# Performance work log

Measured on AMD Instinct MI355X. Metric: run time of the kernel, lower is better.

The kernel has to match this reference:

```python
import jax, jax.numpy as jnp
import numpy as np

N_NODES = 100000
IN_FEAT = 256
OUT_FEAT = 128
N_EDGES = 3200000


def setup_inputs() -> dict:
    key = jax.random.key(0)
    k1, k2, k3, k4, k5 = jax.random.split(key, 5)
    inputs = jax.random.normal(k1, (N_NODES, IN_FEAT), dtype=jnp.float32)
    # xavier-uniform-like init for weight
    limit = float(np.sqrt(6.0 / (IN_FEAT + OUT_FEAT)))
    weight = jax.random.uniform(k2, (IN_FEAT, OUT_FEAT), dtype=jnp.float32, minval=-limit, maxval=limit)
    adj_rows = jnp.sort(jax.random.randint(k3, (N_EDGES,), 0, N_NODES, dtype=jnp.int64))
    adj_cols = jax.random.randint(k4, (N_EDGES,), 0, N_NODES, dtype=jnp.int64)
    adj_vals = jax.random.uniform(k5, (N_EDGES,), dtype=jnp.float32)
    return {"inputs": inputs, "weight": weight, "adj_rows": adj_rows,
            "adj_cols": adj_cols, "adj_vals": adj_vals}


def reference(inputs, weight, adj_rows, adj_cols, adj_vals):
    # support = X @ W  -> [N, out_features]
    support = jnp.matmul(inputs, weight)
    # output = spmm(A, support): out[r] += vals[e] * support[cols[e]] for row r = rows[e]
    gathered = adj_vals[:, None] * support[adj_cols]  # [E, out_features]
    output = jax.ops.segment_sum(gathered, adj_rows, num_segments=N_NODES)
    return output
```

## Files before the change

kernel.cpp:

```cpp
#include <hip/hip_runtime.h>

#define IN_FEAT 256
#define OUT_FEAT 128

typedef __attribute__((ext_vector_type(8))) short bf16x8;
typedef __attribute__((ext_vector_type(4))) float f32x4;

static __device__ __forceinline__ unsigned short f2bf(float f) {
    union { float f; unsigned u; } v; v.f = f;
    unsigned u = v.u;
    return (unsigned short)((u + 0x7FFFu + ((u >> 16) & 1u)) >> 16);
}
static __device__ __forceinline__ float bfl(unsigned u) {
    union { unsigned u; float f; } x; x.u = u << 16; return x.f;
}
static __device__ __forceinline__ float bfh(unsigned u) {
    union { unsigned u; float f; } x; x.u = u & 0xFFFF0000u; return x.f;
}

__global__ __launch_bounds__(256) void prep_wt(const float* __restrict__ W,
                                               unsigned short* __restrict__ Wt) {
    int idx = blockIdx.x * 256 + threadIdx.x;
    int n = idx >> 8, k = idx & 255;
    Wt[idx] = f2bf(W[(size_t)k * OUT_FEAT + n]);
}

__global__ __launch_bounds__(256) void rowptr_kernel(const int* __restrict__ rows,
                                                     int* __restrict__ row_ptr,
                                                     int E, int N) {
    int i = blockIdx.x * 256 + threadIdx.x;
    if (i > N) return;
    int lo = 0, hi = E;
    while (lo < hi) {
        int mid = (lo + hi) >> 1;
        if (rows[mid] < i) lo = mid + 1; else hi = mid;
    }
    row_ptr[i] = lo;
}

__global__ __launch_bounds__(256) void gemm_bf16(const float* __restrict__ X,
                                                 const unsigned short* __restrict__ Wt,
                                                 unsigned short* __restrict__ S, int M) {
    __shared__ unsigned short As[128 * 64];
    __shared__ unsigned short Bs[128 * 64];

    const int t = threadIdx.x;
    const int m0 = blockIdx.x * 128;
    const int lane = t & 63;
    const int w = t >> 6;
    const int wm = w >> 1, wn = w & 1;
    const int lr = lane & 15, lg = lane >> 4;

    f32x4 acc[4][4];
#pragma unroll
    for (int mi = 0; mi < 4; ++mi)
#pragma unroll
        for (int ni = 0; ni < 4; ++ni)
            acc[mi][ni] = (f32x4){0.f, 0.f, 0.f, 0.f};

    const int r_st = t >> 1;
    const int h_st = t & 1;

    for (int k0 = 0; k0 < IN_FEAT; k0 += 64) {
        int gr = m0 + r_st; if (gr >= M) gr = M - 1;
        const float4* xp = (const float4*)(X + (size_t)gr * IN_FEAT + k0 + h_st * 32);
#pragma unroll
        for (int j = 0; j < 4; ++j) {
            float4 f0 = xp[2 * j], f1 = xp[2 * j + 1];
            uint4 pk;
            pk.x = (unsigned)f2bf(f0.x) | ((unsigned)f2bf(f0.y) << 16);
            pk.y = (unsigned)f2bf(f0.z) | ((unsigned)f2bf(f0.w) << 16);
            pk.z = (unsigned)f2bf(f1.x) | ((unsigned)f2bf(f1.y) << 16);
            pk.w = (unsigned)f2bf(f1.z) | ((unsigned)f2bf(f1.w) << 16);
            int s = h_st * 4 + j;
            *(uint4*)((char*)As + r_st * 128 + ((s ^ (r_st & 7)) << 4)) = pk;
        }
        const uint4* wp = (const uint4*)(Wt + (size_t)r_st * 256 + k0 + h_st * 32);
#pragma unroll
        for (int j = 0; j < 4; ++j) {
            uint4 pk = wp[j];
            int s = h_st * 4 + j;
            *(uint4*)((char*)Bs + r_st * 128 + ((s ^ (r_st & 7)) << 4)) = pk;
        }
        __syncthreads();

#pragma unroll
        for (int kb = 0; kb < 2; ++kb) {
            const int sb = kb * 4 + lg;
            bf16x8 a[4], b[4];
#pragma unroll
            for (int mi = 0; mi < 4; ++mi) {
                int r = wm * 64 + mi * 16 + lr;
                a[mi] = *(const bf16x8*)((const char*)As + r * 128 + ((sb ^ (r & 7)) << 4));
            }
#pragma unroll
            for (int ni = 0; ni < 4; ++ni) {
                int r = wn * 64 + ni * 16 + lr;
                b[ni] = *(const bf16x8*)((const char*)Bs + r * 128 + ((sb ^ (r & 7)) << 4));
            }
#pragma unroll
            for (int mi = 0; mi < 4; ++mi)
#pragma unroll
                for (int ni = 0; ni < 4; ++ni)
                    acc[mi][ni] = __builtin_amdgcn_mfma_f32_16x16x32_bf16(a[mi], b[ni], acc[mi][ni], 0, 0, 0);
        }
        __syncthreads();
    }

#pragma unroll
    for (int mi = 0; mi < 4; ++mi) {
#pragma unroll
        for (int j = 0; j < 4; ++j) {
            int row = m0 + wm * 64 + mi * 16 + lg * 4 + j;
            if (row < M) {
#pragma unroll
                for (int ni = 0; ni < 4; ++ni) {
                    int col = wn * 64 + ni * 16 + lr;
                    S[(size_t)row * OUT_FEAT + col] = f2bf(acc[mi][ni][j]);
                }
            }
        }
    }
}

__global__ __launch_bounds__(256) void spmm_bf16(const int* __restrict__ cols,
                                                 const float* __restrict__ vals,
                                                 const unsigned short* __restrict__ S,
                                                 const int* __restrict__ row_ptr,
                                                 float* __restrict__ out, int N) {
    const int w = threadIdx.x >> 6;
    const int lane = threadIdx.x & 63;
    const int r = blockIdx.x * 4 + w;
    if (r >= N) return;
    const int g = lane >> 4;
    const int fb = lane & 15;
    const int start = row_ptr[r], end = row_ptr[r + 1];

    float acc[8] = {0.f, 0.f, 0.f, 0.f, 0.f, 0.f, 0.f, 0.f};
    const unsigned short* Sb = S + fb * 8;

    for (int base = start; base < end; base += 8) {
        int e0 = base + g;
        int e1 = base + 4 + g;
        if (e0 < end) {
            int c = cols[e0]; float v = vals[e0];
            uint4 p = *(const uint4*)(Sb + (size_t)c * OUT_FEAT);
            acc[0] += v * bfl(p.x); acc[1] += v * bfh(p.x);
            acc[2] += v * bfl(p.y); acc[3] += v * bfh(p.y);
            acc[4] += v * bfl(p.z); acc[5] += v * bfh(p.z);
            acc[6] += v * bfl(p.w); acc[7] += v * bfh(p.w);
        }
        if (e1 < end) {
            int c = cols[e1]; float v = vals[e1];
            uint4 p = *(const uint4*)(Sb + (size_t)c * OUT_FEAT);
            acc[0] += v * bfl(p.x); acc[1] += v * bfh(p.x);
            acc[2] += v * bfl(p.y); acc[3] += v * bfh(p.y);
            acc[4] += v * bfl(p.z); acc[5] += v * bfh(p.z);
            acc[6] += v * bfl(p.w); acc[7] += v * bfh(p.w);
        }
    }

#pragma unroll
    for (int j = 0; j < 8; ++j) {
        acc[j] += __shfl_xor(acc[j], 16);
        acc[j] += __shfl_xor(acc[j], 32);
    }
    if (g == 0) {
        float4 o0 = make_float4(acc[0], acc[1], acc[2], acc[3]);
        float4 o1 = make_float4(acc[4], acc[5], acc[6], acc[7]);
        *(float4*)(out + (size_t)r * OUT_FEAT + fb * 8) = o0;
        *(float4*)(out + (size_t)r * OUT_FEAT + fb * 8 + 4) = o1;
    }
}

extern "C" void kernel_launch(void* const* d_in, const int* in_sizes, int n_in,
                              void* d_out, int out_size, void* d_ws, size_t ws_size,
                              hipStream_t stream) {
    const float* X    = (const float*)d_in[0];
    const float* W    = (const float*)d_in[1];
    const int*   rows = (const int*)d_in[2];
    const int*   cols = (const int*)d_in[3];
    const float* vals = (const float*)d_in[4];
    float*       out  = (float*)d_out;

    const int M = in_sizes[0] / IN_FEAT;
    const int E = in_sizes[2];

    unsigned short* S  = (unsigned short*)d_ws;
    unsigned short* Wt = S + (size_t)M * OUT_FEAT;
    int* row_ptr = (int*)(Wt + IN_FEAT * OUT_FEAT);

    prep_wt<<<(IN_FEAT * OUT_FEAT) / 256, 256, 0, stream>>>(W, Wt);
    rowptr_kernel<<<(M + 256) / 256 + 1, 256, 0, stream>>>(rows, row_ptr, E, M);
    gemm_bf16<<<(M + 127) / 128, 256, 0, stream>>>(X, Wt, S, M);
    spmm_bf16<<<(M + 3) / 4, 256, 0, stream>>>(cols, vals, S, row_ptr, out, M);
}
```

Measured before the change: 328.1 us.

## Keep full W tile in LDS for GEMM and batch gathers in SpMM

The GEMM now loads the whole 128x256 bf16 weight matrix into shared memory once per block. Each of 8 warps streams its own 16 rows of X straight from global memory into MFMA operands, so the per-k-step A staging and barriers go away. Output tiles are staged through LDS so the global stores are coalesced 16-byte writes. The SpMM loop is unrolled to issue four independent row gathers per lane before accumulating, which raises memory-level parallelism, at the cost of 64KB LDS per GEMM block and clamped redundant loads at row ends.

```diff
diff --git a/kernel.cpp b/kernel.cpp
--- a/kernel.cpp
+++ b/kernel.cpp
@@ -38,88 +38,61 @@
     row_ptr[i] = lo;
 }
 
-__global__ __launch_bounds__(256) void gemm_bf16(const float* __restrict__ X,
-                                                 const unsigned short* __restrict__ Wt,
-                                                 unsigned short* __restrict__ S, int M) {
-    __shared__ unsigned short As[128 * 64];
-    __shared__ unsigned short Bs[128 * 64];
+__global__ __launch_bounds__(512, 4) void gemm_v3(const float* __restrict__ X,
+                                                  const unsigned short* __restrict__ Wt,
+                                                  unsigned short* __restrict__ S, int M) {
+    __shared__ unsigned short Bs[128 * 256];
 
-    const int t = threadIdx.x;
+    for (int i = threadIdx.x; i < 4096; i += 512) {
+        int r = i >> 5, s = i & 31;
+        ((uint4*)Bs)[(r << 5) | (s ^ (r & 7))] = ((const uint4*)Wt)[i];
+    }
+    __syncthreads();
+
+    const int w = threadIdx.x >> 6;
+    const int lane = threadIdx.x & 63;
+    const int lr = lane & 15, lg = lane >> 4;
     const int m0 = blockIdx.x * 128;
-    const int lane = t & 63;
-    const int w = t >> 6;
-    const int wm = w >> 1, wn = w & 1;
-    const int lr = lane & 15, lg = lane >> 4;
+    const int row = m0 + w * 16 + lr;
+    const int crow = (row < M) ? row : (M - 1);
+    const float4* xp = (const float4*)(X + (size_t)crow * IN_FEAT) + lg * 2;
 
-    f32x4 acc[4][4];
+    f32x4 acc[8];
 #pragma unroll
-    for (int mi = 0; mi < 4; ++mi)
-#pragma unroll
-        for (int ni = 0; ni < 4; ++ni)
-            acc[mi][ni] = (f32x4){0.f, 0.f, 0.f, 0.f};
-
-    const int r_st = t >> 1;
-    const int h_st = t & 1;
-
-    for (int k0 = 0; k0 < IN_FEAT; k0 += 64) {
-        int gr = m0 + r_st; if (gr >= M) gr = M - 1;
-        const float4* xp = (const float4*)(X + (size_t)gr * IN_FEAT + k0 + h_st * 32);
-#pragma unroll
-        for (int j = 0; j < 4; ++j) {
-            float4 f0 = xp[2 * j], f1 = xp[2 * j + 1];
-            uint4 pk;
-            pk.x = (unsigned)f2bf(f0.x) | ((unsigned)f2bf(f0.y) << 16);
-            pk.y = (unsigned)f2bf(f0.z) | ((unsigned)f2bf(f0.w) << 16);
-            pk.z = (unsigned)f2bf(f1.x) | ((unsigned)f2bf(f1.y) << 16);
-            pk.w = (unsigned)f2bf(f1.z) | ((unsigned)f2bf(f1.w) << 16);
-            int s = h_st * 4 + j;
-            *(uint4*)((char*)As + r_st * 128 + ((s ^ (r_st & 7)) << 4)) = pk;
-        }
-        const uint4* wp = (const uint4*)(Wt + (size_t)r_st * 256 + k0 + h_st * 32);
-#pragma unroll
-        for (int j = 0; j < 4; ++j) {
-            uint4 pk = wp[j];
-            int s = h_st * 4 + j;
-            *(uint4*)((char*)Bs + r_st * 128 + ((s ^ (r_st & 7)) << 4)) = pk;
-        }
-        __syncthreads();
+    for (int ni = 0; ni < 8; ++ni) acc[ni] = (f32x4){0.f, 0.f, 0.f, 0.f};
 
 #pragma unroll
-        for (int kb = 0; kb < 2; ++kb) {
-            const int sb = kb * 4 + lg;
-            bf16x8 a[4], b[4];
+    for (int kb = 0; kb < 8; ++kb) {
+        float4 f0 = xp[kb * 8];
+        float4 f1 = xp[kb * 8 + 1];
+        union { uint4 u; bf16x8 v; } a;
+        a.u.x = (unsigned)f2bf(f0.x) | ((unsigned)f2bf(f0.y) << 16);
+        a.u.y = (unsigned)f2bf(f0.z) | ((unsigned)f2bf(f0.w) << 16);
+        a.u.z = (unsigned)f2bf(f1.x) | ((unsigned)f2bf(f1.y) << 16);
+        a.u.w = (unsigned)f2bf(f1.z) | ((unsigned)f2bf(f1.w) << 16);
+        const int sb = kb * 4 + lg;
 #pragma unroll
-            for (int mi = 0; mi < 4; ++mi) {
-                int r = wm * 64 + mi * 16 + lr;
-                a[mi] = *(const bf16x8*)((const char*)As + r * 128 + ((sb ^ (r & 7)) << 4));
-            }
-#pragma unroll
-            for (int ni = 0; ni < 4; ++ni) {
-                int r = wn * 64 + ni * 16 + lr;
-                b[ni] = *(const bf16x8*)((const char*)Bs + r * 128 + ((sb ^ (r & 7)) << 4));
-            }
-#pragma unroll
-            for (int mi = 0; mi < 4; ++mi)
-#pragma unroll
-                for (int ni = 0; ni < 4; ++ni)
-                    acc[mi][ni] = __builtin_amdgcn_mfma_f32_16x16x32_bf16(a[mi], b[ni], acc[mi][ni], 0, 0, 0);
+        for (int ni = 0; ni < 8; ++ni) {
+            int r2 = ni * 16 + lr;
+            bf16x8 b = ((const bf16x8*)Bs)[(r2 << 5) | (sb ^ (r2 & 7))];
+            acc[ni] = __builtin_amdgcn_mfma_f32_16x16x32_bf16(a.v, b, acc[ni], 0, 0, 0);
         }
-        __syncthreads();
     }
 
+    __syncthreads();
+    unsigned short* Cs = Bs + w * 16 * 128;
 #pragma unroll
-    for (int mi = 0; mi < 4; ++mi) {
+    for (int ni = 0; ni < 8; ++ni)
 #pragma unroll
-        for (int j = 0; j < 4; ++j) {
-            int row = m0 + wm * 64 + mi * 16 + lg * 4 + j;
-            if (row < M) {
-#pragma unroll
-                for (int ni = 0; ni < 4; ++ni) {
-                    int col = wn * 64 + ni * 16 + lr;
-                    S[(size_t)row * OUT_FEAT + col] = f2bf(acc[mi][ni][j]);
-                }
-            }
-        }
+        for (int j = 0; j < 4; ++j)
+            Cs[(lg * 4 + j) * 128 + ni * 16 + lr] = f2bf(acc[ni][j]);
+    __syncthreads();
+
+    const int rows_blk = (M - m0 < 128) ? (M - m0) : 128;
+    for (int i = threadIdx.x; i < 2048; i += 512) {
+        int R = i >> 4;
+        if (R < rows_blk)
+            ((uint4*)(S + (size_t)(m0 + R) * OUT_FEAT))[i & 15] = ((const uint4*)Bs)[i];
     }
 }
 
@@ -139,24 +112,25 @@
     float acc[8] = {0.f, 0.f, 0.f, 0.f, 0.f, 0.f, 0.f, 0.f};
     const unsigned short* Sb = S + fb * 8;
 
-    for (int base = start; base < end; base += 8) {
-        int e0 = base + g;
-        int e1 = base + 4 + g;
-        if (e0 < end) {
-            int c = cols[e0]; float v = vals[e0];
-            uint4 p = *(const uint4*)(Sb + (size_t)c * OUT_FEAT);
-            acc[0] += v * bfl(p.x); acc[1] += v * bfh(p.x);
-            acc[2] += v * bfl(p.y); acc[3] += v * bfh(p.y);
-            acc[4] += v * bfl(p.z); acc[5] += v * bfh(p.z);
-            acc[6] += v * bfl(p.w); acc[7] += v * bfh(p.w);
+    for (int base = start; base < end; base += 16) {
+        int   c[4]; float v[4]; uint4 p[4];
+#pragma unroll
+        for (int u = 0; u < 4; ++u) {
+            int e = base + u * 4 + g;
+            int ec = (e < end) ? e : (end - 1);
+            c[u] = cols[ec];
+            v[u] = (e < end) ? vals[ec] : 0.f;
         }
-        if (e1 < end) {
-            int c = cols[e1]; float v = vals[e1];
-            uint4 p = *(const uint4*)(Sb + (size_t)c * OUT_FEAT);
-            acc[0] += v * bfl(p.x); acc[1] += v * bfh(p.x);
-            acc[2] += v * bfl(p.y); acc[3] += v * bfh(p.y);
-            acc[4] += v * bfl(p.z); acc[5] += v * bfh(p.z);
-            acc[6] += v * bfl(p.w); acc[7] += v * bfh(p.w);
+#pragma unroll
+        for (int u = 0; u < 4; ++u)
+            p[u] = *(const uint4*)(Sb + (size_t)c[u] * OUT_FEAT);
+#pragma unroll
+        for (int u = 0; u < 4; ++u) {
+            float v0 = v[u];
+            acc[0] += v0 * bfl(p[u].x); acc[1] += v0 * bfh(p[u].x);
+            acc[2] += v0 * bfl(p[u].y); acc[3] += v0 * bfh(p[u].y);
+            acc[4] += v0 * bfl(p[u].z); acc[5] += v0 * bfh(p[u].z);
+            acc[6] += v0 * bfl(p[u].w); acc[7] += v0 * bfh(p[u].w);
         }
     }
 
@@ -166,10 +140,10 @@
         acc[j] += __shfl_xor(acc[j], 32);
     }
     if (g == 0) {
-        float4 o0 = make_float4(acc[0], acc[1], acc[2], acc[3]);
-        float4 o1 = make_float4(acc[4], acc[5], acc[6], acc[7]);
-        *(float4*)(out + (size_t)r * OUT_FEAT + fb * 8) = o0;
-        *(float4*)(out + (size_t)r * OUT_FEAT + fb * 8 + 4) = o1;
+        *(float4*)(out + (size_t)r * OUT_FEAT + fb * 8) =
+            make_float4(acc[0], acc[1], acc[2], acc[3]);
+        *(float4*)(out + (size_t)r * OUT_FEAT + fb * 8 + 4) =
+            make_float4(acc[4], acc[5], acc[6], acc[7]);
     }
 }
 
@@ -192,6 +166,6 @@
 
     prep_wt<<<(IN_FEAT * OUT_FEAT) / 256, 256, 0, stream>>>(W, Wt);
     rowptr_kernel<<<(M + 256) / 256 + 1, 256, 0, stream>>>(rows, row_ptr, E, M);
-    gemm_bf16<<<(M + 127) / 128, 256, 0, stream>>>(X, Wt, S, M);
+    gemm_v3<<<(M + 127) / 128, 512, 0, stream>>>(X, Wt, S, M);
     spmm_bf16<<<(M + 3) / 4, 256, 0, stream>>>(cols, vals, S, row_ptr, out, M);
 }
```

Result: faster. 310.0 us (-5.5%).
